# Optimization experiments

Hardware: AMD Instinct MI355X
Metric: run time of the kernel (lower is better)

Reference implementation:

```python
import jax, jax.numpy as jnp
import numpy as np

B, H, W, C = 32, 56, 56, 512
WS, SHIFT, NH = 7, 3, 16
HID = 4 * C
EPS = 1e-5


def layernorm(x, g, b):
    m = jnp.mean(x, axis=-1, keepdims=True)
    v = jnp.mean(jnp.square(x - m), axis=-1, keepdims=True)
    return (x - m) * jax.lax.rsqrt(v + EPS) * g + b


def setup_inputs() -> dict:
    key = jax.random.key(0)
    ks = jax.random.split(key, 16)
    s = 0.02
    return {
        "x": jax.random.normal(ks[0], (B, H * W, C), jnp.float32),
        "wqkv": jax.random.normal(ks[1], (3 * C, C), jnp.float32) * s,
        "bqkv": jnp.zeros((3 * C,), jnp.float32),
        "wo": jax.random.normal(ks[2], (C, C), jnp.float32) * s,
        "bo": jnp.zeros((C,), jnp.float32),
        "g1": jnp.ones((C,), jnp.float32),
        "b1": jnp.zeros((C,), jnp.float32),
        "g2": jnp.ones((C,), jnp.float32),
        "b2": jnp.zeros((C,), jnp.float32),
        "w_mlp1": jax.random.normal(ks[3], (HID, C), jnp.float32) * s,
        "b_mlp1": jnp.zeros((HID,), jnp.float32),
        "w_mlp2": jax.random.normal(ks[4], (C, HID), jnp.float32) * s,
        "b_mlp2": jnp.zeros((C,), jnp.float32),
    }


def window_partition(x4):
    # (B,H,W,C) -> (B*nW, WS*WS, C)
    x = x4.reshape(B, H // WS, WS, W // WS, WS, C)
    return x.transpose(0, 1, 3, 2, 4, 5).reshape(-1, WS * WS, C)


def window_reverse(win):
    # (B*nW, WS*WS, C) -> (B,H,W,C)
    x = win.reshape(B, H // WS, W // WS, WS, WS, C)
    return x.transpose(0, 1, 3, 2, 4, 5).reshape(B, H, W, C)


def mha(xn, wqkv, bqkv, wo, bo):
    NW, T, _ = xn.shape
    Dh = C // NH
    qkv = xn @ wqkv.T + bqkv                      # (NW, T, 3C)
    q, k, v = jnp.split(qkv, 3, axis=-1)
    sh = lambda t: t.reshape(NW, T, NH, Dh).transpose(0, 2, 1, 3)  # (NW,NH,T,Dh)
    q, k, v = sh(q), sh(k), sh(v)
    scores = jnp.einsum('whqd,whkd->whqk', q, k) * (Dh ** -0.5)
    a = jax.nn.softmax(scores, axis=-1)
    o = jnp.einsum('whqk,whkd->whqd', a, v).transpose(0, 2, 1, 3).reshape(NW, T, C)
    return o @ wo.T + bo


def reference(x, wqkv, bqkv, wo, bo, g1, b1, g2, b2, w_mlp1, b_mlp1, w_mlp2, b_mlp2):
    x4 = x.reshape(B, H, W, C)
    shifted = jnp.roll(x4, (-SHIFT, -SHIFT), axis=(1, 2))
    win = window_partition(shifted)               # (B*64, 49, C)
    shortcut = win
    wn = layernorm(win, g1, b1)
    attn = mha(wn, wqkv, bqkv, wo, bo)
    win = shortcut + attn
    _ = window_reverse(win)  # NOTE: discarded, faithfully matching the source (x is rebuilt from shifted_x)
    xr = jnp.roll(shifted, (SHIFT, SHIFT), axis=(1, 2)).reshape(B, H * W, C)
    h = layernorm(xr, g2, b2)
    h = jax.nn.gelu(h @ w_mlp1.T + b_mlp1, approximate=False) @ w_mlp2.T + b_mlp2
    return xr + h
```

## Files before the change

### kernel.cpp

```cpp
#include <hip/hip_runtime.h>
#include <hip/hip_bf16.h>
#include <cstdint>
#include <cstddef>

#define MROWS 100352
#define CDIM  512
#define HDIM  2048

typedef __attribute__((ext_vector_type(8))) short   short8;
typedef __attribute__((ext_vector_type(8))) __bf16  bf16x8;
typedef __attribute__((ext_vector_type(4))) __bf16  bf16x4;
typedef __attribute__((ext_vector_type(4))) float   floatx4;

static __device__ __forceinline__ unsigned short f2bf(float f) {
  union { float f; unsigned int u; } c; c.f = f;
  unsigned int u = c.u;
  return (unsigned short)((u + 0x7FFFu + ((u >> 16) & 1u)) >> 16);
}

static __device__ __forceinline__ void gload_lds16(const void* g, void* l) {
  __builtin_amdgcn_global_load_lds(
      (const __attribute__((address_space(1))) void*)g,
      (__attribute__((address_space(3))) void*)l, 16, 0, 0);
}

#define BAR()   asm volatile("s_barrier" ::: "memory")
#define LGKM0() asm volatile("s_waitcnt lgkmcnt(0)" ::: "memory")
#define VMC0()  asm volatile("s_waitcnt vmcnt(0)" ::: "memory")

__global__ void cast_weights(const float4* __restrict__ s1, unsigned short* __restrict__ d1,
                             const float4* __restrict__ s2, unsigned short* __restrict__ d2) {
  int t = blockIdx.x * 256 + threadIdx.x;
  const int N4 = (HDIM * CDIM) / 4;
  const float4* s; unsigned short* d; int idx;
  if (t < N4) { s = s1; d = d1; idx = t; }
  else        { s = s2; d = d2; idx = t - N4; }
  float4 f = s[idx];
  ushort4 u = make_ushort4(f2bf(f.x), f2bf(f.y), f2bf(f.z), f2bf(f.w));
  *reinterpret_cast<ushort4*>(d + (size_t)idx * 4) = u;
}

__global__ void ln_cast(const float* __restrict__ x, const float* __restrict__ g,
                        const float* __restrict__ b, unsigned short* __restrict__ xn) {
  const int row  = blockIdx.x * 4 + (threadIdx.x >> 6);
  const int lane = threadIdx.x & 63;
  const float4* xr = reinterpret_cast<const float4*>(x + (size_t)row * CDIM);
  const float4 v0 = xr[lane], v1 = xr[lane + 64];
  float s  = v0.x + v0.y + v0.z + v0.w + v1.x + v1.y + v1.z + v1.w;
  float ss = v0.x*v0.x + v0.y*v0.y + v0.z*v0.z + v0.w*v0.w
           + v1.x*v1.x + v1.y*v1.y + v1.z*v1.z + v1.w*v1.w;
#pragma unroll
  for (int o = 1; o < 64; o <<= 1) { s += __shfl_xor(s, o); ss += __shfl_xor(ss, o); }
  const float mean = s * (1.0f / CDIM);
  const float rstd = rsqrtf(ss * (1.0f / CDIM) - mean * mean + 1e-5f);
  const float4* g4 = reinterpret_cast<const float4*>(g);
  const float4* b4 = reinterpret_cast<const float4*>(b);
  const float4 ga = g4[lane], gb = g4[lane + 64];
  const float4 ba = b4[lane], bb = b4[lane + 64];
  ushort4 o0 = make_ushort4(
      f2bf((v0.x - mean) * rstd * ga.x + ba.x),
      f2bf((v0.y - mean) * rstd * ga.y + ba.y),
      f2bf((v0.z - mean) * rstd * ga.z + ba.z),
      f2bf((v0.w - mean) * rstd * ga.w + ba.w));
  ushort4 o1 = make_ushort4(
      f2bf((v1.x - mean) * rstd * gb.x + bb.x),
      f2bf((v1.y - mean) * rstd * gb.y + bb.y),
      f2bf((v1.z - mean) * rstd * gb.z + bb.z),
      f2bf((v1.w - mean) * rstd * gb.w + bb.w));
  unsigned short* orow = xn + (size_t)row * CDIM;
  *reinterpret_cast<ushort4*>(orow + lane * 4)        = o0;
  *reinterpret_cast<ushort4*>(orow + (lane + 64) * 4) = o1;
}

template<int KDIM, int NDIM, int EPI>
__global__ __launch_bounds__(256, 2) void gemm128(
    const unsigned short* __restrict__ A, const unsigned short* __restrict__ Bw,
    const float* __restrict__ bias, const float* __restrict__ resid,
    void* __restrict__ Cout) {
  constexpr int nt = KDIM / 64;
  __shared__ __align__(16) unsigned short smA[2][8192];
  __shared__ __align__(16) unsigned short smB[2][8192];

  const int tid  = threadIdx.x;
  const int lane = tid & 63, w = tid >> 6;
  const int swr = w >> 1, swc = w & 1;
  const int frow = lane & 15, fk = (lane >> 4) * 8;

  constexpr int GX = NDIM / 128;
  const int nwg = gridDim.x;
  const int lid = ((int)blockIdx.x & 7) * (nwg >> 3) + ((int)blockIdx.x >> 3);
  const int m0 = (lid / GX) * 128, n0 = (lid % GX) * 128;

  const size_t ldb = (size_t)KDIM * 2;
  const int srow = tid >> 3;
  const int scb  = ((tid ^ (tid >> 3)) & 7) * 16;
  const char* gA = (const char*)A  + (size_t)(m0 + srow) * ldb + scb;
  const char* gB = (const char*)Bw + (size_t)(n0 + srow) * ldb + scb;

  auto STG = [&](int t, int buf) {
    const char* sa = gA + (size_t)t * 128;
    const char* sb = gB + (size_t)t * 128;
#pragma unroll
    for (int j = 0; j < 4; ++j)
      gload_lds16(sa + (size_t)j * 32 * ldb, &smA[buf][j * 2048 + w * 512]);
#pragma unroll
    for (int j = 0; j < 4; ++j)
      gload_lds16(sb + (size_t)j * 32 * ldb, &smB[buf][j * 2048 + w * 512]);
  };

  floatx4 acc[4][4] = {};

  STG(0, 0);
  VMC0();
  BAR();

  for (int t = 0; t < nt; ++t) {
    const int p = t & 1;
    bf16x8 a[8], b[8];
#pragma unroll
    for (int mi = 0; mi < 4; ++mi)
#pragma unroll
      for (int kk = 0; kk < 2; ++kk) {
        const int row = swr * 64 + mi * 16 + frow;
        const int col = kk * 32 + fk;
        a[mi * 2 + kk] = __builtin_bit_cast(bf16x8,
            *reinterpret_cast<const short8*>(
                &smA[p][row * 64 + (col ^ ((row & 7) << 3))]));
      }
#pragma unroll
    for (int nj = 0; nj < 4; ++nj)
#pragma unroll
      for (int kk = 0; kk < 2; ++kk) {
        const int row = swc * 64 + nj * 16 + frow;
        const int col = kk * 32 + fk;
        b[nj * 2 + kk] = __builtin_bit_cast(bf16x8,
            *reinterpret_cast<const short8*>(
                &smB[p][row * 64 + (col ^ ((row & 7) << 3))]));
      }

    if (t + 1 < nt) STG(t + 1, p ^ 1);

    __builtin_amdgcn_s_setprio(1);
#pragma unroll
    for (int mi = 0; mi < 4; ++mi)
#pragma unroll
      for (int nj = 0; nj < 4; ++nj)
#pragma unroll
        for (int kk = 0; kk < 2; ++kk)
          acc[mi][nj] = __builtin_amdgcn_mfma_f32_16x16x32_bf16(
              b[nj * 2 + kk], a[mi * 2 + kk], acc[mi][nj], 0, 0, 0);
    __builtin_amdgcn_s_setprio(0);

    if (t + 1 < nt) {
      LGKM0();
      VMC0();
      BAR();
    }
  }

  const int em = lane & 15;
  const int en = (lane >> 4) << 2;

  float4 bj[4];
#pragma unroll
  for (int nj = 0; nj < 4; ++nj)
    bj[nj] = *reinterpret_cast<const float4*>(&bias[n0 + swc * 64 + nj * 16 + en]);

#pragma unroll
  for (int mi = 0; mi < 4; ++mi) {
    const int gm = m0 + swr * 64 + mi * 16 + em;
    const size_t rowoff = (size_t)gm * NDIM + n0 + swc * 64 + en;
#pragma unroll
    for (int nj = 0; nj < 4; ++nj) {
      const float4 bb = bj[nj];
      const floatx4 av = acc[mi][nj];
      float v0 = av[0] + bb.x, v1 = av[1] + bb.y;
      float v2 = av[2] + bb.z, v3 = av[3] + bb.w;
      const size_t off = rowoff + nj * 16;
      if (EPI == 1) {
        v0 *= __builtin_amdgcn_rcpf(1.0f + __expf(-1.702f * v0));
        v1 *= __builtin_amdgcn_rcpf(1.0f + __expf(-1.702f * v1));
        v2 *= __builtin_amdgcn_rcpf(1.0f + __expf(-1.702f * v2));
        v3 *= __builtin_amdgcn_rcpf(1.0f + __expf(-1.702f * v3));
        bf16x4 o = { (__bf16)v0, (__bf16)v1, (__bf16)v2, (__bf16)v3 };
        *reinterpret_cast<bf16x4*>((unsigned short*)Cout + off) = o;
      } else {
        const float4 r4 = *reinterpret_cast<const float4*>(resid + off);
        float4 o = make_float4(v0 + r4.x, v1 + r4.y, v2 + r4.z, v3 + r4.w);
        *reinterpret_cast<float4*>((float*)Cout + off) = o;
      }
    }
  }
}

extern "C" void kernel_launch(void* const* d_in, const int* in_sizes, int n_in,
                              void* d_out, int out_size, void* d_ws, size_t ws_size,
                              hipStream_t stream) {
  const float* x   = (const float*)d_in[0];
  const float* g2  = (const float*)d_in[7];
  const float* b2  = (const float*)d_in[8];
  const float* w1  = (const float*)d_in[9];
  const float* b1  = (const float*)d_in[10];
  const float* w2  = (const float*)d_in[11];
  const float* b2m = (const float*)d_in[12];
  float* out = (float*)d_out;


  unsigned short* w1b = (unsigned short*)d_ws;
  unsigned short* w2b = w1b + (size_t)HDIM * CDIM;
  unsigned short* G   = w2b + (size_t)HDIM * CDIM;
  unsigned short* xn = (unsigned short*)d_out;

  cast_weights<<<2048, 256, 0, stream>>>((const float4*)w1, w1b, (const float4*)w2, w2b);
  ln_cast<<<MROWS / 4, 256, 0, stream>>>(x, g2, b2, xn);

  gemm128<CDIM, HDIM, 1>
      <<<dim3((MROWS / 128) * (HDIM / 128)), 256, 0, stream>>>(
          xn, w1b, b1, nullptr, (void*)G);

  gemm128<HDIM, CDIM, 2>
      <<<dim3((MROWS / 128) * (CDIM / 128)), 256, 0, stream>>>(
          G, w2b, b2m, x, (void*)out);
}
```

Measured before the change: 743.4 us.

## Replace double-buffered K=64 GEMM pipeline with single-buffer K=32 at higher occupancy

The GEMM kernel drops the double-buffered LDS prefetch and now loads one K=32 tile per iteration into a single smaller buffer. Each iteration waits for that load before computing. LDS use per block falls to a quarter and the launch bounds ask for 4 blocks per CU instead of 2, so latency is meant to be hidden by more resident waves rather than by software prefetch. The cost is a full load-wait-barrier round trip for every K step, twice as many iterations, and no overlap between loading and compute inside a block.

Result: faster. 695.8 us (-6.4%).

```diff
diff --git a/kernel.cpp b/kernel.cpp
--- a/kernel.cpp
+++ b/kernel.cpp
@@ -25,7 +25,6 @@
 }
 
 #define BAR()   asm volatile("s_barrier" ::: "memory")
-#define LGKM0() asm volatile("s_waitcnt lgkmcnt(0)" ::: "memory")
 #define VMC0()  asm volatile("s_waitcnt vmcnt(0)" ::: "memory")
 
 __global__ void cast_weights(const float4* __restrict__ s1, unsigned short* __restrict__ d1,
@@ -73,18 +72,18 @@
 }
 
 template<int KDIM, int NDIM, int EPI>
-__global__ __launch_bounds__(256, 2) void gemm128(
+__global__ __launch_bounds__(256, 4) void gemm_m97(
     const unsigned short* __restrict__ A, const unsigned short* __restrict__ Bw,
     const float* __restrict__ bias, const float* __restrict__ resid,
     void* __restrict__ Cout) {
-  constexpr int nt = KDIM / 64;
-  __shared__ __align__(16) unsigned short smA[2][8192];
-  __shared__ __align__(16) unsigned short smB[2][8192];
+  constexpr int nt = KDIM / 32;
+  __shared__ __align__(16) unsigned short smA[128 * 32];
+  __shared__ __align__(16) unsigned short smB[128 * 32];
 
   const int tid  = threadIdx.x;
   const int lane = tid & 63, w = tid >> 6;
   const int swr = w >> 1, swc = w & 1;
-  const int frow = lane & 15, fk = (lane >> 4) * 8;
+  const int frow = lane & 15, fslot = lane >> 4;
 
   constexpr int GX = NDIM / 128;
   const int nwg = gridDim.x;
@@ -92,74 +91,56 @@
   const int m0 = (lid / GX) * 128, n0 = (lid % GX) * 128;
 
   const size_t ldb = (size_t)KDIM * 2;
-  const int srow = tid >> 3;
-  const int scb  = ((tid ^ (tid >> 3)) & 7) * 16;
+  const int srow = tid >> 2;
+  const int scb  = ((tid ^ (tid >> 2)) & 3) * 16;
   const char* gA = (const char*)A  + (size_t)(m0 + srow) * ldb + scb;
   const char* gB = (const char*)Bw + (size_t)(n0 + srow) * ldb + scb;
 
-  auto STG = [&](int t, int buf) {
-    const char* sa = gA + (size_t)t * 128;
-    const char* sb = gB + (size_t)t * 128;
-#pragma unroll
-    for (int j = 0; j < 4; ++j)
-      gload_lds16(sa + (size_t)j * 32 * ldb, &smA[buf][j * 2048 + w * 512]);
-#pragma unroll
-    for (int j = 0; j < 4; ++j)
-      gload_lds16(sb + (size_t)j * 32 * ldb, &smB[buf][j * 2048 + w * 512]);
+  auto STG = [&](int kt) {
+    const char* sa = gA + (size_t)kt * 64;
+    const char* sb = gB + (size_t)kt * 64;
+    gload_lds16(sa,                  &smA[tid * 8]);
+    gload_lds16(sa + 64 * ldb,       &smA[2048 + tid * 8]);
+    gload_lds16(sb,                  &smB[tid * 8]);
+    gload_lds16(sb + 64 * ldb,       &smB[2048 + tid * 8]);
   };
 
   floatx4 acc[4][4] = {};
 
-  STG(0, 0);
-  VMC0();
-  BAR();
-
-  for (int t = 0; t < nt; ++t) {
-    const int p = t & 1;
-    bf16x8 a[8], b[8];
+  for (int kt = 0; kt < nt; ++kt) {
+    if (kt > 0) BAR();
+    STG(kt);
+    VMC0();
+    BAR();
+
+    bf16x8 a[4], b[4];
+#pragma unroll
+    for (int mi = 0; mi < 4; ++mi) {
+      const int row = swr * 64 + mi * 16 + frow;
+      const int sl  = fslot ^ (row & 3);
+      a[mi] = __builtin_bit_cast(bf16x8,
+          *reinterpret_cast<const short8*>(&smA[row * 32 + sl * 8]));
+    }
+#pragma unroll
+    for (int nj = 0; nj < 4; ++nj) {
+      const int row = swc * 64 + nj * 16 + frow;
+      const int sl  = fslot ^ (row & 3);
+      b[nj] = __builtin_bit_cast(bf16x8,
+          *reinterpret_cast<const short8*>(&smB[row * 32 + sl * 8]));
+    }
+
+    __builtin_amdgcn_s_setprio(1);
 #pragma unroll
     for (int mi = 0; mi < 4; ++mi)
 #pragma unroll
-      for (int kk = 0; kk < 2; ++kk) {
-        const int row = swr * 64 + mi * 16 + frow;
-        const int col = kk * 32 + fk;
-        a[mi * 2 + kk] = __builtin_bit_cast(bf16x8,
-            *reinterpret_cast<const short8*>(
-                &smA[p][row * 64 + (col ^ ((row & 7) << 3))]));
-      }
-#pragma unroll
-    for (int nj = 0; nj < 4; ++nj)
-#pragma unroll
-      for (int kk = 0; kk < 2; ++kk) {
-        const int row = swc * 64 + nj * 16 + frow;
-        const int col = kk * 32 + fk;
-        b[nj * 2 + kk] = __builtin_bit_cast(bf16x8,
-            *reinterpret_cast<const short8*>(
-                &smB[p][row * 64 + (col ^ ((row & 7) << 3))]));
-      }
-
-    if (t + 1 < nt) STG(t + 1, p ^ 1);
-
-    __builtin_amdgcn_s_setprio(1);
-#pragma unroll
-    for (int mi = 0; mi < 4; ++mi)
-#pragma unroll
       for (int nj = 0; nj < 4; ++nj)
-#pragma unroll
-        for (int kk = 0; kk < 2; ++kk)
-          acc[mi][nj] = __builtin_amdgcn_mfma_f32_16x16x32_bf16(
-              b[nj * 2 + kk], a[mi * 2 + kk], acc[mi][nj], 0, 0, 0);
+        acc[mi][nj] = __builtin_amdgcn_mfma_f32_16x16x32_bf16(
+            b[nj], a[mi], acc[mi][nj], 0, 0, 0);
     __builtin_amdgcn_s_setprio(0);
-
-    if (t + 1 < nt) {
-      LGKM0();
-      VMC0();
-      BAR();
-    }
   }
 
   const int em = lane & 15;
-  const int en = (lane >> 4) << 2;
+  const int en = fslot << 2;
 
   float4 bj[4];
 #pragma unroll
@@ -214,11 +195,11 @@
   cast_weights<<<2048, 256, 0, stream>>>((const float4*)w1, w1b, (const float4*)w2, w2b);
   ln_cast<<<MROWS / 4, 256, 0, stream>>>(x, g2, b2, xn);
 
-  gemm128<CDIM, HDIM, 1>
+  gemm_m97<CDIM, HDIM, 1>
       <<<dim3((MROWS / 128) * (HDIM / 128)), 256, 0, stream>>>(
           xn, w1b, b1, nullptr, (void*)G);
 
-  gemm128<HDIM, CDIM, 2>
+  gemm_m97<HDIM, CDIM, 2>
       <<<dim3((MROWS / 128) * (CDIM / 128)), 256, 0, stream>>>(
           G, w2b, b2m, x, (void*)out);
 }
```
